# Kernel optimization log

Hardware: AMD Instinct MI355X
Metric: run time of the kernel (lower is better)

## Reference

```python
import jax, jax.numpy as jnp
import numpy as np

C = 32768          # camera rays
B = 64             # batch
N = 2 * C          # nodes
E = 3 * C - 2      # edges (h1: C-1, h2: C-1, v: C)


def _edge_index(c):
    h1 = np.vstack([np.arange(0, c - 1), np.arange(1, c)])
    h2 = np.vstack([np.arange(c, 2 * c - 1), np.arange(c + 1, 2 * c)])
    v = np.vstack([np.arange(0, c), np.arange(c, 2 * c)])
    return np.hstack([h1, h2, v]).astype(np.int32)  # (2, E): row0=src(j), row1=dst(i)


def _linear_init(k, out_f, in_f):
    k1, k2 = jax.random.split(k)
    s = 1.0 / np.sqrt(in_f)
    w = jax.random.uniform(k1, (out_f, in_f), minval=-s, maxval=s, dtype=jnp.float32)
    b = jax.random.uniform(k2, (out_f,), minval=-s, maxval=s, dtype=jnp.float32)
    return w, b


def setup_inputs() -> dict:
    key = jax.random.key(0)
    ks = jax.random.split(key, 10)
    ei = _edge_index(C)
    w1a, b1a = _linear_init(ks[2], 4, 8)
    w1b, b1b = _linear_init(ks[3], 4, 4)
    w2a, b2a = _linear_init(ks[4], 8, 12)
    w2b, b2b = _linear_init(ks[5], 8, 8)
    w3a, b3a = _linear_init(ks[6], 16, 20)
    w3b, b3b = _linear_init(ks[7], 16, 16)
    wmu, bmu = _linear_init(ks[8], 1, 32)
    return {
        "x": jax.random.normal(ks[0], (B, N, 2), dtype=jnp.float32),
        "e": jax.random.normal(ks[1], (B, E, 4), dtype=jnp.float32),
        "src": jnp.asarray(ei[0]),
        "dst": jnp.asarray(ei[1]),
        "w1a": w1a, "b1a": b1a, "w1b": w1b, "b1b": b1b,
        "w2a": w2a, "b2a": b2a, "w2b": w2b, "b2b": b2b,
        "w3a": w3a, "b3a": b3a, "w3b": w3b, "b3b": b3b,
        "wmu": wmu, "bmu": bmu,
    }


def _edge_conv(x, e, src, dst, w1, b1, w2, b2):
    # x: (B, N, F_in), e: (B, E, 4) -> (B, N, F_out)
    x_i = x[:, dst, :]                                   # central node feats (B, E, F_in)
    x_j = x[:, src, :]                                   # neighbor feats     (B, E, F_in)
    m = jnp.concatenate([x_i, x_j, e], axis=-1)          # (B, E, 2*F_in+4)
    m = jax.nn.relu(jnp.einsum('bef,of->beo', m, w1) + b1)
    m = jnp.einsum('bef,of->beo', m, w2) + b2            # (B, E, F_out)
    # scatter-max into target nodes; empty segments -> 0 (PyG zero-fill)
    agg = jax.vmap(lambda mb: jax.ops.segment_max(mb, dst, num_segments=N))(m)
    return jnp.where(jnp.isneginf(agg), 0.0, agg)


def reference(x, e, src, dst,
              w1a, b1a, w1b, b1b,
              w2a, b2a, w2b, b2b,
              w3a, b3a, w3b, b3b,
              wmu, bmu):
    h = _edge_conv(x, e, src, dst, w1a, b1a, w1b, b1b)   # (B, N, 4)
    h = _edge_conv(h, e, src, dst, w2a, b2a, w2b, b2b)   # (B, N, 8)
    h = _edge_conv(h, e, src, dst, w3a, b3a, w3b, b3b)   # (B, N, 16)
    h = jnp.concatenate([h[:, :C, :], h[:, C:, :]], axis=-1)  # (B, C, 32)
    mu = (jnp.einsum('bcf,of->bco', h, wmu) + bmu)[..., 0]    # (B, C) = Normal loc, scale=1
    return mu
```

## Files before the change

kernel.cpp:

```cpp
#include <hip/hip_runtime.h>
#include <cstdint>

#define GC 32768
#define GN (2*GC)
#define GE (3*GC-2)
#define NSTRIP 1024

typedef _Float16 f16x8 __attribute__((ext_vector_type(8)));
typedef float f32x4 __attribute__((ext_vector_type(4)));

__device__ __forceinline__ float g1w(const float* w1, int F, int H, int f, int n) {
    if (n >= 3 * H) return 0.f;
    int t = n / H, h = n % H;
    const float* w = w1 + h * (2 * F + 4);
    if (t == 0) {
        if (f < F) return w[f];
        if (f >= 2*F && f < 3*F) return w[F + f - 2*F];
        if (f >= 4*F && f < 4*F + 4) return w[2*F + f - 4*F];
    } else if (t == 1) {
        if (f >= F && f < 2*F) return w[f - F];
        if (f >= 3*F && f < 4*F) return w[F + f - 3*F];
        if (f >= 4*F + 4 && f < 4*F + 8) return w[2*F + f - (4*F+4)];
    } else {
        if (f < F) return w[F + f];
        if (f >= F && f < 2*F) return w[f - F];
        if (f >= 4*F + 8 && f < 4*F + 12) return w[2*F + f - (4*F+8)];
    }
    return 0.f;
}

__device__ __forceinline__ uint32_t pkf16(float a, float b) {
    unsigned short ua = __builtin_bit_cast(unsigned short, (_Float16)a);
    unsigned short ub = __builtin_bit_cast(unsigned short, (_Float16)b);
    return (uint32_t)ua | ((uint32_t)ub << 16);
}
__device__ __forceinline__ uint32_t splitpk(float v) {
    _Float16 h = (_Float16)v;
    _Float16 lo = (_Float16)(v - (float)h);
    return (uint32_t)__builtin_bit_cast(unsigned short, h) |
           ((uint32_t)__builtin_bit_cast(unsigned short, lo) << 16);
}
template<int CTRL>
__device__ __forceinline__ float dppadd(float v) {
    int s = __builtin_amdgcn_update_dpp(0, __builtin_bit_cast(int, v),
                                        CTRL, 0xF, 0xF, true);
    return v + __builtin_bit_cast(float, s);
}

__global__ void build_frags(const float* __restrict__ w1a, const float* __restrict__ w1b,
                            const float* __restrict__ w2a, const float* __restrict__ w2b,
                            const float* __restrict__ w3a, const float* __restrict__ w3b,
                            uint4* __restrict__ tab) {
    int tid = blockIdx.x * 256 + threadIdx.x;
    if (tid >= 11 * 64) return;
    int fr = tid >> 6, l = tid & 63;
    int col = l & 15, kq = l >> 4;
    float v[8];
#pragma unroll
    for (int i = 0; i < 8; ++i) {
        int kin = kq * 8 + i;
        int f = kin >> 1;
        float val = 0.f;
        if (fr < 2)        val = g1w(w1a, 2, 4, (fr * 32 + kin) >> 1, col);
        else if (fr == 2)  val = (kin < 4 && col < 4) ? w1b[col * 4 + kin] : 0.f;
        else if (fr < 7)  { int nt = (fr - 3) >> 1, c = (fr - 3) & 1;
                            if (c == 0)
                                val = (kin < 16) ? g1w(w2a, 4, 8, kin, nt * 16 + col) : 0.f;
                            else
                                val = g1w(w2a, 4, 8, (32 + kin) >> 1, nt * 16 + col); }
        else if (fr == 7)  val = (kin < 8 && col < 8) ? w2b[col * 8 + kin] : 0.f;
        else if (fr == 8)  val = (kin < 16) ? w3a[col * 20 + kin] : 0.f;
        else if (fr == 9)  val = (f < 4)  ? w3a[col * 20 + 16 + f] : 0.f;
        else               val = (kin < 16) ? w3b[col * 16 + kin] : 0.f;
        v[i] = val;
    }
    uint4 o;
    o.x = pkf16(v[0], v[1]); o.y = pkf16(v[2], v[3]);
    o.z = pkf16(v[4], v[5]); o.w = pkf16(v[6], v[7]);
    tab[fr * 64 + l] = o;
}

#define OFF_E   0
#define OFF_X   96
#define OFF_H2  128
#define OFF_H3  192
#define OFF_Z1  272
#define OFF_Z2  320
#define OFF_Z3  384
#define ROWB    496
#define OUTSTRIDE 132
#define OUTWAVE   (16*OUTSTRIDE)

__device__ __forceinline__ f32x4 mfma16(uint4 a, uint4 b, f32x4 c) {
    return __builtin_amdgcn_mfma_f32_16x16x32_f16(
        __builtin_bit_cast(f16x8, a), __builtin_bit_cast(f16x8, b), c, 0, 0, 0);
}

#define PR4(r) _Pragma("unroll") for (int r = 0; r < 4; ++r)

#define BODY(C, P, W, DO_L12, DO_L3, DO_CMT) do {                                  \
    const int itv = 4*(W) + (C);                                                   \
    if (DO_L3) {                                                                   \
        const bool jp3 = FIRST ? ((j0 + itv - 3) >= 1) : true;                     \
        f32x4 s0 = mfma16(*(const uint4*)rADS[0][(P)^1], BF[8], zero);             \
        s0 = mfma16(*(const uint4*)rAEp[0][P], BF[9], s0);                         \
        f32x4 s1 = mfma16(*(const uint4*)rADS[1][(P)^1], BF[8], zero);             \
        s1 = mfma16(*(const uint4*)rAEp[1][P], BF[9], s1);                         \
        f32x4 s2 = mfma16(*(const uint4*)rADS[2][(P)^1], BF[8], zero);             \
        s2 = mfma16(*(const uint4*)rAEp[2][P], BF[9], s2);                         \
        PR4(r) { *(_Float16*)(wZ3 +  0 + r*ROWB) = (_Float16)fmaxf(s0[r]+zb3,0.f); \
                 *(_Float16*)(wZ3 + 32 + r*ROWB) = (_Float16)fmaxf(s1[r]+zb3,0.f); \
                 *(_Float16*)(wZ3 + 64 + r*ROWB) = (_Float16)fmaxf(s2[r]+zb3,0.f); }\
        f32x4 g0 = mfma16(*(const uint4*)rZ3t[0], BF[10], zero);                   \
        f32x4 g1 = mfma16(*(const uint4*)rZ3t[1], BF[10], zero);                   \
        f32x4 g2 = mfma16(*(const uint4*)rZ3t[2], BF[10], zero);                   \
        float part[4];                                                             \
        PR4(r) { float h0 = jp3 ? g0[r] + cb3 : 0.f;                               \
                 float h1 = (jp3 ? fmaxf(g1[r], g2[r]) : g2[r]) + cb3;             \
                 part[r] = fmaf(h0, wm0, h1 * wm1); }                              \
        PR4(r) { part[r] = dppadd<0xB1>(part[r]);                                  \
                 part[r] = dppadd<0x4E>(part[r]);                                  \
                 part[r] = dppadd<0x141>(part[r]);                                 \
                 part[r] = dppadd<0x140>(part[r]); }                               \
        if (n < 4) {                                                               \
            float v = part[0];                                                     \
            v = (n == 1) ? part[1] : v;                                            \
            v = (n == 2) ? part[2] : v;                                            \
            v = (n == 3) ? part[3] : v;                                            \
            *(float*)(outw + (itv - 3) * 4) = v + bm;                              \
        }                                                                          \
    }                                                                              \
    if (DO_L12) {                                                                  \
        const bool jp = FIRST ? ((j0 + itv - 2) >= 1) : true;                      \
        uint4 a0 = *(const uint4*)rA0p[P];                                         \
        uint4 a1 = *(const uint4*)rA1p[P];                                         \
        f32x4 d1 = mfma16(a0, BF[0], zero); d1 = mfma16(a1, BF[1], d1);            \
        if (n < 12) { PR4(r) *(_Float16*)(wZ1t + r*ROWB) =                         \
                          (_Float16)fmaxf(d1[r] + zb1, 0.f); }                     \
        f32x4 dt0 = mfma16(*(const uint4*)(rZ1 +  0), BF[2], zero);                \
        f32x4 dt1 = mfma16(*(const uint4*)(rZ1 + 16), BF[2], zero);                \
        f32x4 dt2 = mfma16(*(const uint4*)(rZ1 + 32), BF[2], zero);                \
        if (n < 4) { PR4(r) {                                                      \
            float h0 = jp ? dt0[r] + cb1 : 0.f;                                    \
            float h1 = (jp ? fmaxf(dt1[r], dt2[r]) : dt2[r]) + cb1;                \
            *(_Float16*)(wH2p[P] + r*ROWB)     = (_Float16)h0;                     \
            *(_Float16*)(wH2p[P] + 8 + r*ROWB) = (_Float16)h1; } }                 \
        uint4 b0 = *(const uint4*)rB0p[P];                                         \
        uint4 b1 = *(const uint4*)rB1p[P];                                         \
        f32x4 t0 = mfma16(b0, BF[3], zero); t0 = mfma16(b1, BF[4], t0);            \
        f32x4 t1 = mfma16(b0, BF[5], zero); t1 = mfma16(b1, BF[6], t1);            \
        PR4(r) *(_Float16*)(wZ2n + r*ROWB) = (_Float16)fmaxf(t0[r] + zb2, 0.f);    \
        if (n < 8) { PR4(r) *(_Float16*)(wZ2n + 32 + r*ROWB) =                     \
                         (_Float16)fmaxf(t1[r] + zb2, 0.f); }                      \
        f32x4 u0 = mfma16(*(const uint4*)rZ2r[0], BF[7], zero);                    \
        f32x4 u1 = mfma16(*(const uint4*)rZ2r[1], BF[7], zero);                    \
        f32x4 u2 = mfma16(*(const uint4*)rZ2r[2], BF[7], zero);                    \
        if (n < 8) { PR4(r) {                                                      \
            float h0 = jp ? u0[r] + cb2 : 0.f;                                     \
            float h1 = (jp ? fmaxf(u1[r], u2[r]) : u2[r]) + cb2;                   \
            *(_Float16*)(wH3p[P] + r*ROWB)      = (_Float16)h0;                    \
            *(_Float16*)(wH3p[P] + 16 + r*ROWB) = (_Float16)h1; } }                \
    }                                                                              \
    if (DO_CMT) {                                                                  \
        float4 val;                                                                \
        if (q < 3) val = ck[C];                                                    \
        else val = make_float4(                                                    \
            ((C)&1) ? ck[(C)>>1].z     : ck[(C)>>1].x,                             \
            ((C)&1) ? ck[(C)>>1].w     : ck[(C)>>1].y,                             \
            ((C)&1) ? ck[2+((C)>>1)].z : ck[2+((C)>>1)].x,                         \
            ((C)&1) ? ck[2+((C)>>1)].w : ck[2+((C)>>1)].y );                       \
        uint4 o; o.x = splitpk(val.x); o.y = splitpk(val.y);                       \
        o.z = splitpk(val.z); o.w = splitpk(val.w);                                \
        if (q < 3) *(uint4*)cmtpE[P] = o;                                          \
        else       *(uint4*)cmtpX[P] = o;                                          \
    }                                                                              \
} while (0)

template<bool FIRST>
__device__ __forceinline__ void mfma_body(
    const float* __restrict__ x, const float* __restrict__ e,
    const float* __restrict__ b1a, const float* __restrict__ b1b,
    const float* __restrict__ b2a, const float* __restrict__ b2b,
    const float* __restrict__ b3a, const float* __restrict__ b3b,
    const float* __restrict__ wmu, const float* __restrict__ bmu,
    const uint4* __restrict__ tab, float* __restrict__ out,
    char* smem, int strip)
{
    const int l  = threadIdx.x & 63;
    const int wv = threadIdx.x >> 6;
    char* wbase  = smem + wv * 16 * ROWB;
    char* ldsout = smem + 4 * 16 * ROWB + wv * OUTWAVE;

    const int bg = wv;
    const int j0 = strip * 32;

    const int n = l & 15;
    const int q = l >> 4;

    {
        uint32_t* p = (uint32_t*)wbase;
#pragma unroll
        for (int i = 0; i < 31; ++i) p[l * 31 + i] = 0u;
    }

    uint4 BF[11];
#pragma unroll
    for (int f = 0; f < 11; ++f) BF[f] = tab[f * 64 + l];

    const float zb1 = b1a[n & 3], zb2 = b2a[n & 7], zb3 = b3a[n];
    const float cb1 = b1b[n & 3], cb2 = b2b[n & 7], cb3 = b3b[n];
    const float wm0 = wmu[n], wm1 = wmu[16 + n];
    const float bm  = bmu[0];

    const int mB = bg * 16 + n;
    const size_t xrow = (size_t)mB * GN * 2;
    const size_t erow = (size_t)mB * GE * 4;

    char* rr = wbase + n * ROWB;
    char* wr = wbase + (q * 4) * ROWB;
    const f32x4 zero = {0.f, 0.f, 0.f, 0.f};

    const float* eb_ptr = e + erow + (q == 0 ? 0 : q == 1 ? (size_t)(GC - 1) * 4
                                                          : (size_t)(2 * (GC - 1)) * 4);
    const int posoff = (q == 2 ? 1 : 0) - 2;
    const float* xp0 = x + xrow;
    const float* xp1 = x + xrow + (size_t)2 * GC;

    char *rA0p[2], *rA1p[2], *rB0p[2], *rB1p[2], *wH2p[2], *wH3p[2];
    char *cmtpE[2], *cmtpX[2];
    char *rAEp[3][2], *rADS[3][2], *rZ2r[3], *rZ3t[3];
#pragma unroll
    for (int pp = 0; pp < 2; ++pp) {
        rA0p[pp] = rr + (q == 0 ? OFF_X + pp * 16 : q == 1 ? OFF_X + (pp ^ 1) * 16
                        : q == 2 ? OFF_E + pp * 48 : OFF_E + pp * 48 + 16);
        rA1p[pp] = rr + OFF_E + pp * 48 + (q == 0 ? 32 : 0);
        rB0p[pp] = rr + (q == 0 ? OFF_H2 + pp * 16
                        : q == 1 ? OFF_H2 + (pp ^ 1) * 16 : OFF_H2 + 32);
        rB1p[pp] = rr + OFF_E + pp * 48 + (q == 0 ? 0 : q == 1 ? 16 : q == 2 ? 32 : 0);
        wH2p[pp] = wr + OFF_H2 + pp * 16 + n * 2;
        wH3p[pp] = wr + OFF_H3 + pp * 32 + n * 2;
        cmtpE[pp] = rr + OFF_E + (pp ^ 1) * 48 + q * 16;
        cmtpX[pp] = rr + OFF_X + (pp ^ 1) * 16;
#pragma unroll
        for (int t = 0; t < 3; ++t) {
            rAEp[t][pp] = rr + OFF_E + (pp ^ 1) * 48 + (q == 0 ? t * 16 : 0);
            int offq0 = (t == 0) ? OFF_H3 + pp * 32 : OFF_H3 + pp * 32 + 16;
            int offq1 = (t == 0) ? OFF_H3 + (pp ^ 1) * 32
                      : (t == 1) ? OFF_H3 + (pp ^ 1) * 32 + 16
                                 : OFF_H3 + pp * 32;
            rADS[t][pp] = rr + (q == 0 ? offq0 : q == 1 ? offq1 : OFF_H3 + 64);
        }
    }
#pragma unroll
    for (int t = 0; t < 3; ++t) {
        rZ2r[t] = rr + OFF_Z2 + (q == 0 ? t * 16 : 48);
        rZ3t[t] = (q < 2) ? rr + OFF_Z3 + t * 32 + q * 16 : rr + OFF_H3 + 64;
    }
    char* wZ1t = wr + OFF_Z1 + (n >> 2) * 16 + (n & 3) * 2;
    char* rZ1  = rr + OFF_Z1;
    char* wZ2n = wr + OFF_Z2 + n * 2;
    char* wZ3  = wr + OFF_Z3 + n * 2;
    char* outw = ldsout + (q * 4 + n) * OUTSTRIDE;

    float4 ck[4];

    if (q < 3) {
        int P = min(max(j0 - 3 + (q == 2 ? 1 : 0), 0), (q == 2 ? GC - 1 : GC - 2));
        float4 ev = *(const float4*)(eb_ptr + 4 * (size_t)P);
        uint4 o; o.x = splitpk(ev.x); o.y = splitpk(ev.y);
        o.z = splitpk(ev.z); o.w = splitpk(ev.w);
        *(uint4*)(rr + OFF_E + q * 16) = o;
    } else {
#pragma unroll
        for (int s = 0; s < 2; ++s) {
            int P = min(max(j0 - 3 + s, 0), GC - 1);
            float2 a = *(const float2*)(xp0 + 2 * (size_t)P);
            float2 b = *(const float2*)(xp1 + 2 * (size_t)P);
            uint4 o; o.x = splitpk(a.x); o.y = splitpk(a.y);
            o.z = splitpk(b.x); o.w = splitpk(b.y);
            *(uint4*)(rr + OFF_X + (1 - s) * 16) = o;
        }
    }

    if (q < 3) {
#pragma unroll
        for (int cc = 0; cc < 4; ++cc) {
            int P = min(max(j0 + cc + posoff, 0), (q == 2 ? GC - 1 : GC - 2));
            ck[cc] = *(const float4*)(eb_ptr + 4 * (size_t)P);
        }
    } else {
#pragma unroll
        for (int cc = 0; cc < 4; ++cc) {
            int P = min(max(j0 - 1 + cc, 0), GC - 1);
            float2 a = *(const float2*)(xp0 + 2 * (size_t)P);
            float2 b = *(const float2*)(xp1 + 2 * (size_t)P);
            if (cc == 0)      { ck[0].x=a.x; ck[0].y=a.y; ck[2].x=b.x; ck[2].y=b.y; }
            else if (cc == 1) { ck[0].z=a.x; ck[0].w=a.y; ck[2].z=b.x; ck[2].w=b.y; }
            else if (cc == 2) { ck[1].x=a.x; ck[1].y=a.y; ck[3].x=b.x; ck[3].y=b.y; }
            else              { ck[1].z=a.x; ck[1].w=a.y; ck[3].z=b.x; ck[3].w=b.y; }
        }
    }
    BODY(0, 0, 0, true, false, true);
    BODY(1, 1, 0, true, false, true);
    BODY(2, 0, 0, true, false, true);
    BODY(3, 1, 0, true, true,  true);

    for (int w = 1; w < 8; ++w) {
        if (q < 3) {
            const float* pe = eb_ptr + 4 * (size_t)(j0 + 4 * w + posoff);
            ck[0] = *(const float4*)(pe);
            ck[1] = *(const float4*)(pe + 4);
            ck[2] = *(const float4*)(pe + 8);
            ck[3] = *(const float4*)(pe + 12);
        } else {
            const float* p0 = xp0 + 2 * (size_t)(j0 + 4 * w - 1);
            const float* p1 = xp1 + 2 * (size_t)(j0 + 4 * w - 1);
            ck[0].x = p0[0]; ck[0].y = p0[1]; ck[0].z = p0[2]; ck[0].w = p0[3];
            ck[1].x = p0[4]; ck[1].y = p0[5]; ck[1].z = p0[6]; ck[1].w = p0[7];
            ck[2].x = p1[0]; ck[2].y = p1[1]; ck[2].z = p1[2]; ck[2].w = p1[3];
            ck[3].x = p1[4]; ck[3].y = p1[5]; ck[3].z = p1[6]; ck[3].w = p1[7];
        }
        BODY(0, 0, w, true, true, true);
        BODY(1, 1, w, true, true, true);
        BODY(2, 0, w, true, true, true);
        BODY(3, 1, w, true, true, true);
    }

    if (q < 3) {
#pragma unroll
        for (int cc = 0; cc < 2; ++cc) {
            int P = min(max(j0 + 32 + cc + posoff, 0), (q == 2 ? GC - 1 : GC - 2));
            ck[cc] = *(const float4*)(eb_ptr + 4 * (size_t)P);
        }
    } else {
#pragma unroll
        for (int cc = 0; cc < 2; ++cc) {
            int P = min(max(j0 + 31 + cc, 0), GC - 1);
            float2 a = *(const float2*)(xp0 + 2 * (size_t)P);
            float2 b = *(const float2*)(xp1 + 2 * (size_t)P);
            if (cc == 0) { ck[0].x=a.x; ck[0].y=a.y; ck[2].x=b.x; ck[2].y=b.y; }
            else         { ck[0].z=a.x; ck[0].w=a.y; ck[2].z=b.x; ck[2].w=b.y; }
        }
    }
    BODY(0, 0, 8, true, true, true);
    BODY(1, 1, 8, true, true, true);
    BODY(2, 0, 8, false, true, false);

    {
        const int bl = l >> 2, cc = l & 3;
        char* orow = ldsout + bl * OUTSTRIDE + cc * 32;
        float4 v0 = *(const float4*)(orow);
        float4 v1 = *(const float4*)(orow + 16);
        float* ob = out + (size_t)(bg * 16 + bl) * GC + j0 + cc * 8;
        *(float4*)(ob)     = v0;
        *(float4*)(ob + 4) = v1;
    }
}

__global__ __launch_bounds__(256, 4) void gnn_mfma(
    const float* __restrict__ x, const float* __restrict__ e,
    const float* __restrict__ b1a, const float* __restrict__ b1b,
    const float* __restrict__ b2a, const float* __restrict__ b2b,
    const float* __restrict__ b3a, const float* __restrict__ b3b,
    const float* __restrict__ wmu, const float* __restrict__ bmu,
    const uint4* __restrict__ tab, float* __restrict__ out)
{
    __shared__ __align__(16) char smem[4 * 16 * ROWB + 4 * OUTWAVE];
    const int strip = blockIdx.x;
    if (strip == 0)
        mfma_body<true>(x, e, b1a, b1b, b2a, b2b, b3a, b3b, wmu, bmu, tab, out,
                        smem, 0);
    else
        mfma_body<false>(x, e, b1a, b1b, b2a, b2b, b3a, b3b, wmu, bmu, tab, out,
                         smem, strip);
}

extern "C" void kernel_launch(void* const* d_in, const int* in_sizes, int n_in,
                              void* d_out, int out_size, void* d_ws, size_t ws_size,
                              hipStream_t stream) {
    const float* x   = (const float*)d_in[0];
    const float* e   = (const float*)d_in[1];
    const float* w1a = (const float*)d_in[4];
    const float* b1a = (const float*)d_in[5];
    const float* w1b = (const float*)d_in[6];
    const float* b1b = (const float*)d_in[7];
    const float* w2a = (const float*)d_in[8];
    const float* b2a = (const float*)d_in[9];
    const float* w2b = (const float*)d_in[10];
    const float* b2b = (const float*)d_in[11];
    const float* w3a = (const float*)d_in[12];
    const float* b3a = (const float*)d_in[13];
    const float* w3b = (const float*)d_in[14];
    const float* b3b = (const float*)d_in[15];
    const float* wmu = (const float*)d_in[16];
    const float* bmu = (const float*)d_in[17];
    float* out = (float*)d_out;
    uint4* tab = (uint4*)d_ws;

    hipLaunchKernelGGL(build_frags, dim3(3), dim3(256), 0, stream,
                       w1a, w1b, w2a, w2b, w3a, w3b, tab);
    hipLaunchKernelGGL(gnn_mfma, dim3(NSTRIP), dim3(256), 0, stream,
                       x, e, b1a, b1b, b2a, b2b, b3a, b3b, wmu, bmu, tab, out);
}
```

Before: 105.8 us.

## Store edge features as plain fp16 and halve MFMA count per layer

Edge features are now stored in LDS as single fp16 values instead of a hi/lo split pair, which halves their LDS footprint and row stride. The weight fragments are repacked from 11 to 7 so each layer's first linear needs one 16x16x32 MFMA per tile instead of two, and the LDS operand pointers are remapped to match. This cuts MFMA issue, LDS traffic and register use for the B fragments. The cost is lower precision on edge features, since the lo-correction term is dropped, while node features keep the split form.

```diff
diff --git a/kernel.cpp b/kernel.cpp
--- a/kernel.cpp
+++ b/kernel.cpp
@@ -52,26 +52,23 @@
                             const float* __restrict__ w3a, const float* __restrict__ w3b,
                             uint4* __restrict__ tab) {
     int tid = blockIdx.x * 256 + threadIdx.x;
-    if (tid >= 11 * 64) return;
+    if (tid >= 7 * 64) return;
     int fr = tid >> 6, l = tid & 63;
     int col = l & 15, kq = l >> 4;
     float v[8];
 #pragma unroll
     for (int i = 0; i < 8; ++i) {
         int kin = kq * 8 + i;
-        int f = kin >> 1;
         float val = 0.f;
-        if (fr < 2)        val = g1w(w1a, 2, 4, (fr * 32 + kin) >> 1, col);
-        else if (fr == 2)  val = (kin < 4 && col < 4) ? w1b[col * 4 + kin] : 0.f;
-        else if (fr < 7)  { int nt = (fr - 3) >> 1, c = (fr - 3) & 1;
-                            if (c == 0)
-                                val = (kin < 16) ? g1w(w2a, 4, 8, kin, nt * 16 + col) : 0.f;
-                            else
-                                val = g1w(w2a, 4, 8, (32 + kin) >> 1, nt * 16 + col); }
-        else if (fr == 7)  val = (kin < 8 && col < 8) ? w2b[col * 8 + kin] : 0.f;
-        else if (fr == 8)  val = (kin < 16) ? w3a[col * 20 + kin] : 0.f;
-        else if (fr == 9)  val = (f < 4)  ? w3a[col * 20 + 16 + f] : 0.f;
-        else               val = (kin < 16) ? w3b[col * 16 + kin] : 0.f;
+        if (fr == 0) {
+            if (kin < 16)      val = g1w(w1a, 2, 4, kin >> 1, col);
+            else if (kin < 28) val = g1w(w1a, 2, 4, kin - 8, col);
+        }
+        else if (fr == 1) val = (kin < 4 && col < 4) ? w1b[col * 4 + kin] : 0.f;
+        else if (fr < 4)  val = (kin < 28) ? g1w(w2a, 4, 8, kin, (fr - 2) * 16 + col) : 0.f;
+        else if (fr == 4) val = (kin < 8 && col < 8) ? w2b[col * 8 + kin] : 0.f;
+        else if (fr == 5) val = (kin < 20) ? w3a[col * 20 + kin] : 0.f;
+        else              val = (kin < 16) ? w3b[col * 16 + kin] : 0.f;
         v[i] = val;
     }
     uint4 o;
@@ -81,13 +78,13 @@
 }
 
 #define OFF_E   0
-#define OFF_X   96
-#define OFF_H2  128
-#define OFF_H3  192
-#define OFF_Z1  272
-#define OFF_Z2  320
-#define OFF_Z3  384
-#define ROWB    496
+#define OFF_X   64
+#define OFF_H2  96
+#define OFF_H3  128
+#define OFF_Z1  192
+#define OFF_Z2  240
+#define OFF_Z3  288
+#define ROWB    400
 #define OUTSTRIDE 132
 #define OUTWAVE   (16*OUTSTRIDE)
 
@@ -102,18 +99,15 @@
     const int itv = 4*(W) + (C);                                                   \
     if (DO_L3) {                                                                   \
         const bool jp3 = FIRST ? ((j0 + itv - 3) >= 1) : true;                     \
-        f32x4 s0 = mfma16(*(const uint4*)rADS[0][(P)^1], BF[8], zero);             \
-        s0 = mfma16(*(const uint4*)rAEp[0][P], BF[9], s0);                         \
-        f32x4 s1 = mfma16(*(const uint4*)rADS[1][(P)^1], BF[8], zero);             \
-        s1 = mfma16(*(const uint4*)rAEp[1][P], BF[9], s1);                         \
-        f32x4 s2 = mfma16(*(const uint4*)rADS[2][(P)^1], BF[8], zero);             \
-        s2 = mfma16(*(const uint4*)rAEp[2][P], BF[9], s2);                         \
+        f32x4 s0 = mfma16(*(const uint4*)rL3[0][P], BF[5], zero);                  \
+        f32x4 s1 = mfma16(*(const uint4*)rL3[1][P], BF[5], zero);                  \
+        f32x4 s2 = mfma16(*(const uint4*)rL3[2][P], BF[5], zero);                  \
         PR4(r) { *(_Float16*)(wZ3 +  0 + r*ROWB) = (_Float16)fmaxf(s0[r]+zb3,0.f); \
                  *(_Float16*)(wZ3 + 32 + r*ROWB) = (_Float16)fmaxf(s1[r]+zb3,0.f); \
                  *(_Float16*)(wZ3 + 64 + r*ROWB) = (_Float16)fmaxf(s2[r]+zb3,0.f); }\
-        f32x4 g0 = mfma16(*(const uint4*)rZ3t[0], BF[10], zero);                   \
-        f32x4 g1 = mfma16(*(const uint4*)rZ3t[1], BF[10], zero);                   \
-        f32x4 g2 = mfma16(*(const uint4*)rZ3t[2], BF[10], zero);                   \
+        f32x4 g0 = mfma16(*(const uint4*)rZ3t[0], BF[6], zero);                    \
+        f32x4 g1 = mfma16(*(const uint4*)rZ3t[1], BF[6], zero);                    \
+        f32x4 g2 = mfma16(*(const uint4*)rZ3t[2], BF[6], zero);                    \
         float part[4];                                                             \
         PR4(r) { float h0 = jp3 ? g0[r] + cb3 : 0.f;                               \
                  float h1 = (jp3 ? fmaxf(g1[r], g2[r]) : g2[r]) + cb3;             \
@@ -132,29 +126,27 @@
     }                                                                              \
     if (DO_L12) {                                                                  \
         const bool jp = FIRST ? ((j0 + itv - 2) >= 1) : true;                      \
-        uint4 a0 = *(const uint4*)rA0p[P];                                         \
-        uint4 a1 = *(const uint4*)rA1p[P];                                         \
-        f32x4 d1 = mfma16(a0, BF[0], zero); d1 = mfma16(a1, BF[1], d1);            \
+        uint4 a0 = *(const uint4*)rL1[P];                                          \
+        f32x4 d1 = mfma16(a0, BF[0], zero);                                        \
         if (n < 12) { PR4(r) *(_Float16*)(wZ1t + r*ROWB) =                         \
                           (_Float16)fmaxf(d1[r] + zb1, 0.f); }                     \
-        f32x4 dt0 = mfma16(*(const uint4*)(rZ1 +  0), BF[2], zero);                \
-        f32x4 dt1 = mfma16(*(const uint4*)(rZ1 + 16), BF[2], zero);                \
-        f32x4 dt2 = mfma16(*(const uint4*)(rZ1 + 32), BF[2], zero);                \
+        f32x4 dt0 = mfma16(*(const uint4*)(rZ1 +  0), BF[1], zero);                \
+        f32x4 dt1 = mfma16(*(const uint4*)(rZ1 + 16), BF[1], zero);                \
+        f32x4 dt2 = mfma16(*(const uint4*)(rZ1 + 32), BF[1], zero);                \
         if (n < 4) { PR4(r) {                                                      \
             float h0 = jp ? dt0[r] + cb1 : 0.f;                                    \
             float h1 = (jp ? fmaxf(dt1[r], dt2[r]) : dt2[r]) + cb1;                \
             *(_Float16*)(wH2p[P] + r*ROWB)     = (_Float16)h0;                     \
             *(_Float16*)(wH2p[P] + 8 + r*ROWB) = (_Float16)h1; } }                 \
-        uint4 b0 = *(const uint4*)rB0p[P];                                         \
-        uint4 b1 = *(const uint4*)rB1p[P];                                         \
-        f32x4 t0 = mfma16(b0, BF[3], zero); t0 = mfma16(b1, BF[4], t0);            \
-        f32x4 t1 = mfma16(b0, BF[5], zero); t1 = mfma16(b1, BF[6], t1);            \
+        uint4 b0 = *(const uint4*)rL2[P];                                          \
+        f32x4 t0 = mfma16(b0, BF[2], zero);                                        \
+        f32x4 t1 = mfma16(b0, BF[3], zero);                                        \
         PR4(r) *(_Float16*)(wZ2n + r*ROWB) = (_Float16)fmaxf(t0[r] + zb2, 0.f);    \
         if (n < 8) { PR4(r) *(_Float16*)(wZ2n + 32 + r*ROWB) =                     \
                          (_Float16)fmaxf(t1[r] + zb2, 0.f); }                      \
-        f32x4 u0 = mfma16(*(const uint4*)rZ2r[0], BF[7], zero);                    \
-        f32x4 u1 = mfma16(*(const uint4*)rZ2r[1], BF[7], zero);                    \
-        f32x4 u2 = mfma16(*(const uint4*)rZ2r[2], BF[7], zero);                    \
+        f32x4 u0 = mfma16(*(const uint4*)rZ2r[0], BF[4], zero);                    \
+        f32x4 u1 = mfma16(*(const uint4*)rZ2r[1], BF[4], zero);                    \
+        f32x4 u2 = mfma16(*(const uint4*)rZ2r[2], BF[4], zero);                    \
         if (n < 8) { PR4(r) {                                                      \
             float h0 = jp ? u0[r] + cb2 : 0.f;                                     \
             float h1 = (jp ? fmaxf(u1[r], u2[r]) : u2[r]) + cb2;                   \
@@ -169,10 +161,14 @@
             ((C)&1) ? ck[(C)>>1].w     : ck[(C)>>1].y,                             \
             ((C)&1) ? ck[2+((C)>>1)].z : ck[2+((C)>>1)].x,                         \
             ((C)&1) ? ck[2+((C)>>1)].w : ck[2+((C)>>1)].y );                       \
-        uint4 o; o.x = splitpk(val.x); o.y = splitpk(val.y);                       \
-        o.z = splitpk(val.z); o.w = splitpk(val.w);                                \
-        if (q < 3) *(uint4*)cmtpE[P] = o;                                          \
-        else       *(uint4*)cmtpX[P] = o;                                          \
+        if (q < 3) {                                                               \
+            uint2 o2; o2.x = pkf16(val.x, val.y); o2.y = pkf16(val.z, val.w);      \
+            *(uint2*)cmtE[P] = o2;                                                 \
+        } else {                                                                   \
+            uint4 o; o.x = splitpk(val.x); o.y = splitpk(val.y);                   \
+            o.z = splitpk(val.z); o.w = splitpk(val.w);                            \
+            *(uint4*)cmtX[P] = o;                                                  \
+        }                                                                          \
     }                                                                              \
 } while (0)
 
@@ -200,12 +196,12 @@
     {
         uint32_t* p = (uint32_t*)wbase;
 #pragma unroll
-        for (int i = 0; i < 31; ++i) p[l * 31 + i] = 0u;
-    }
-
-    uint4 BF[11];
-#pragma unroll
-    for (int f = 0; f < 11; ++f) BF[f] = tab[f * 64 + l];
+        for (int i = 0; i < 25; ++i) p[l * 25 + i] = 0u;
+    }
+
+    uint4 BF[7];
+#pragma unroll
+    for (int f = 0; f < 7; ++f) BF[f] = tab[f * 64 + l];
 
     const float zb1 = b1a[n & 3], zb2 = b2a[n & 7], zb3 = b3a[n];
     const float cb1 = b1b[n & 3], cb2 = b2b[n & 7], cb3 = b3b[n];
@@ -226,35 +222,39 @@
     const float* xp0 = x + xrow;
     const float* xp1 = x + xrow + (size_t)2 * GC;
 
-    char *rA0p[2], *rA1p[2], *rB0p[2], *rB1p[2], *wH2p[2], *wH3p[2];
-    char *cmtpE[2], *cmtpX[2];
-    char *rAEp[3][2], *rADS[3][2], *rZ2r[3], *rZ3t[3];
+    char *rL1[2], *rL2[2], *rL3[3][2], *wH2p[2], *wH3p[2], *cmtE[2], *cmtX[2];
+    char *rZ2r[3], *rZ3t[3];
 #pragma unroll
     for (int pp = 0; pp < 2; ++pp) {
-        rA0p[pp] = rr + (q == 0 ? OFF_X + pp * 16 : q == 1 ? OFF_X + (pp ^ 1) * 16
-                        : q == 2 ? OFF_E + pp * 48 : OFF_E + pp * 48 + 16);
-        rA1p[pp] = rr + OFF_E + pp * 48 + (q == 0 ? 32 : 0);
-        rB0p[pp] = rr + (q == 0 ? OFF_H2 + pp * 16
-                        : q == 1 ? OFF_H2 + (pp ^ 1) * 16 : OFF_H2 + 32);
-        rB1p[pp] = rr + OFF_E + pp * 48 + (q == 0 ? 0 : q == 1 ? 16 : q == 2 ? 32 : 0);
+        rL1[pp] = rr + (q == 0 ? OFF_X + pp * 16
+                      : q == 1 ? OFF_X + (pp ^ 1) * 16
+                      : q == 2 ? OFF_E + pp * 32
+                               : OFF_E + pp * 32 + 16);
+        rL2[pp] = rr + (q == 0 ? OFF_H2 + pp * 16
+                      : q == 1 ? OFF_H2 + (pp ^ 1) * 16
+                      : q == 2 ? OFF_E + pp * 32
+                               : OFF_E + pp * 32 + 16);
         wH2p[pp] = wr + OFF_H2 + pp * 16 + n * 2;
         wH3p[pp] = wr + OFF_H3 + pp * 32 + n * 2;
-        cmtpE[pp] = rr + OFF_E + (pp ^ 1) * 48 + q * 16;
-        cmtpX[pp] = rr + OFF_X + (pp ^ 1) * 16;
+        cmtE[pp] = rr + OFF_E + (pp ^ 1) * 32 + q * 8;
+        cmtX[pp] = rr + OFF_X + (pp ^ 1) * 16;
 #pragma unroll
         for (int t = 0; t < 3; ++t) {
-            rAEp[t][pp] = rr + OFF_E + (pp ^ 1) * 48 + (q == 0 ? t * 16 : 0);
-            int offq0 = (t == 0) ? OFF_H3 + pp * 32 : OFF_H3 + pp * 32 + 16;
-            int offq1 = (t == 0) ? OFF_H3 + (pp ^ 1) * 32
-                      : (t == 1) ? OFF_H3 + (pp ^ 1) * 32 + 16
-                                 : OFF_H3 + pp * 32;
-            rADS[t][pp] = rr + (q == 0 ? offq0 : q == 1 ? offq1 : OFF_H3 + 64);
+            const int cp = pp ^ 1;
+            int off;
+            if (q == 0)      off = (t == 0) ? OFF_H3 + cp * 32 : OFF_H3 + cp * 32 + 16;
+            else if (q == 1) off = (t == 0) ? OFF_H3 + (cp ^ 1) * 32
+                             : (t == 1) ? OFF_H3 + (cp ^ 1) * 32 + 16
+                                        : OFF_H3 + cp * 32;
+            else if (q == 2) off = OFF_E + cp * 32 + t * 8;
+            else             off = OFF_E;
+            rL3[t][pp] = rr + off;
         }
     }
 #pragma unroll
     for (int t = 0; t < 3; ++t) {
-        rZ2r[t] = rr + OFF_Z2 + (q == 0 ? t * 16 : 48);
-        rZ3t[t] = (q < 2) ? rr + OFF_Z3 + t * 32 + q * 16 : rr + OFF_H3 + 64;
+        rZ2r[t] = rr + OFF_Z2 + (q == 0 ? t * 16 : 0);
+        rZ3t[t] = rr + ((q < 2) ? OFF_Z3 + t * 32 + q * 16 : OFF_Z3);
     }
     char* wZ1t = wr + OFF_Z1 + (n >> 2) * 16 + (n & 3) * 2;
     char* rZ1  = rr + OFF_Z1;
@@ -267,9 +267,8 @@
     if (q < 3) {
         int P = min(max(j0 - 3 + (q == 2 ? 1 : 0), 0), (q == 2 ? GC - 1 : GC - 2));
         float4 ev = *(const float4*)(eb_ptr + 4 * (size_t)P);
-        uint4 o; o.x = splitpk(ev.x); o.y = splitpk(ev.y);
-        o.z = splitpk(ev.z); o.w = splitpk(ev.w);
-        *(uint4*)(rr + OFF_E + q * 16) = o;
+        uint2 o2; o2.x = pkf16(ev.x, ev.y); o2.y = pkf16(ev.z, ev.w);
+        *(uint2*)(rr + OFF_E + q * 8) = o2;
     } else {
 #pragma unroll
         for (int s = 0; s < 2; ++s) {
@@ -397,7 +396,7 @@
     float* out = (float*)d_out;
     uint4* tab = (uint4*)d_ws;
 
-    hipLaunchKernelGGL(build_frags, dim3(3), dim3(256), 0, stream,
+    hipLaunchKernelGGL(build_frags, dim3(2), dim3(256), 0, stream,
                        w1a, w1b, w2a, w2b, w3a, w3b, tab);
     hipLaunchKernelGGL(gnn_mfma, dim3(NSTRIP), dim3(256), 0, stream,
                        x, e, b1a, b1b, b2a, b2b, b3a, b3b, wmu, bmu, tab, out);
```

New measurement: 110.2 us. 4.2% more time.
